# Optimization experiments

Measured on AMD Instinct MI355X. Metric: run time of the kernel, lower is better.

Reference implementation:

```python
import jax, jax.numpy as jnp
import numpy as np

B, T, I, H, L = 32, 512, 512, 512, 2


def gru_dir(x, w_ih, w_hh, b_ih, b_hh):
    """Single-direction GRU over x: [B, T, In] -> [B, T, H]. PyTorch gate order r,z,n."""
    Bb = x.shape[0]
    Hh = w_hh.shape[-1]
    # Fuse input-gate matmuls across all timesteps: [B, T, 3H]
    gx = jnp.einsum('bti,gi->btg', x, w_ih) + b_ih
    gx = jnp.moveaxis(gx, 1, 0)  # [T, B, 3H] for scan

    def step(h, gx_t):
        gh = h @ w_hh.T + b_hh  # [B, 3H]
        xr, xz, xn = jnp.split(gx_t, 3, axis=-1)
        hr, hz, hn = jnp.split(gh, 3, axis=-1)
        r = jax.nn.sigmoid(xr + hr)
        z = jax.nn.sigmoid(xz + hz)
        n = jnp.tanh(xn + r * hn)
        h_new = (1.0 - z) * n + z * h
        return h_new, h_new

    h0 = jnp.zeros((Bb, Hh), x.dtype)
    _, ys = jax.lax.scan(step, h0, gx)
    return jnp.moveaxis(ys, 0, 1)  # [B, T, H]


def bigru_layer(x, w_ih, w_hh, b_ih, b_hh):
    """w_ih: [2, 3H, In]; dir 0 = forward, dir 1 = backward (time-reversed)."""
    fwd = gru_dir(x, w_ih[0], w_hh[0], b_ih[0], b_hh[0])
    bwd = gru_dir(x[:, ::-1], w_ih[1], w_hh[1], b_ih[1], b_hh[1])[:, ::-1]
    return jnp.concatenate([fwd, bwd], axis=-1)  # [B, T, 2H]


def setup_inputs() -> dict:
    key = jax.random.key(0)
    ks = jax.random.split(key, 9)
    k = 1.0 / np.sqrt(H)  # PyTorch default uniform init bound
    u = lambda kk, shape: jax.random.uniform(kk, shape, jnp.float32, -k, k)
    x = jax.random.normal(ks[0], (B, T, I), jnp.float32)
    # Layer 0: input dim I; Layer 1: input dim 2H (bidirectional concat)
    return {
        'x': x,
        'w_ih_l0': u(ks[1], (2, 3 * H, I)),
        'w_hh_l0': u(ks[2], (2, 3 * H, H)),
        'b_ih_l0': u(ks[3], (2, 3 * H)),
        'b_hh_l0': u(ks[4], (2, 3 * H)),
        'w_ih_l1': u(ks[5], (2, 3 * H, 2 * H)),
        'w_hh_l1': u(ks[6], (2, 3 * H, H)),
        'b_ih_l1': u(ks[7], (2, 3 * H)),
        'b_hh_l1': u(ks[8], (2, 3 * H)),
    }


def reference(x, w_ih_l0, w_hh_l0, b_ih_l0, b_hh_l0,
              w_ih_l1, w_hh_l1, b_ih_l1, b_hh_l1):
    h1 = bigru_layer(x, w_ih_l0, w_hh_l0, b_ih_l0[:, None, :].squeeze(1), b_hh_l0)
    out = bigru_layer(h1, w_ih_l1, w_hh_l1, b_ih_l1, b_hh_l1)
    return out  # [B, T, 2H]
```

## Files before the change

kernel.cpp:

```cpp
#include <hip/hip_runtime.h>
#include <hip/hip_bf16.h>
#include <stdint.h>

#define TT 512
#define HD 512
#define BB 32
#define MM (BB*TT)
#define NG 3072
#define WGD 16
#define CPW 32

typedef short short8 __attribute__((ext_vector_type(8)));
typedef float f32x4 __attribute__((ext_vector_type(4)));
typedef float f32x2 __attribute__((ext_vector_type(2)));
typedef unsigned short u16;
typedef unsigned int u32;
typedef unsigned long long u64;

__device__ __forceinline__ u16 f2bf(float f) {
  __hip_bfloat16 h = __float2bfloat16(f);
  union { __hip_bfloat16 h; u16 u; } c; c.h = h; return c.u;
}
__device__ __forceinline__ float bf2f(u16 u) {
  union { u32 i; float f; } c; c.i = ((u32)u) << 16; return c.f;
}
__device__ __forceinline__ float sigmf(float x) {
  return 1.0f / (1.0f + __expf(-x));
}
__device__ __forceinline__ float tanhff(float x) {
  float a = __expf(2.0f * x);
  return 1.0f - 2.0f / (a + 1.0f);
}

__global__ __launch_bounds__(256) void cvt_bf16(const float* __restrict__ in,
                                                u16* __restrict__ out, int n8) {
  int i = blockIdx.x * 256 + threadIdx.x;
  if (i >= n8) return;
  const float4* p = (const float4*)in;
  float4 a = p[2*i], b = p[2*i+1];
  union { short8 v; u16 u[8]; } o;
  o.u[0]=f2bf(a.x); o.u[1]=f2bf(a.y); o.u[2]=f2bf(a.z); o.u[3]=f2bf(a.w);
  o.u[4]=f2bf(b.x); o.u[5]=f2bf(b.y); o.u[6]=f2bf(b.z); o.u[7]=f2bf(b.w);
  ((short8*)out)[i] = o.v;
}

__global__ __launch_bounds__(256) void gemm_gx(const u16* __restrict__ A,
                                               const u16* __restrict__ Bw,
                                               char* __restrict__ gxout,
                                               int K, int gxf32) {
  __shared__ __align__(16) u16 lA[128*32];
  __shared__ __align__(16) u16 lB[128*32];
  const int tid = threadIdx.x;
  const int lane = tid & 63;
  const int wid = tid >> 6;
  const int wr = wid >> 1, wc = wid & 1;
  const int bm = blockIdx.y * 128, bn = blockIdx.x * 128;
  const int col = lane & 15, kg = lane >> 4;

  f32x4 acc[4][4];
#pragma unroll
  for (int m = 0; m < 4; ++m)
#pragma unroll
    for (int n = 0; n < 4; ++n) acc[m][n] = (f32x4){0.f,0.f,0.f,0.f};

  const int nkt = K >> 5;
  for (int kt = 0; kt < nkt; ++kt) {
    short8 ra[2], rb[2];
    const int kb = kt * 32;
#pragma unroll
    for (int p = 0; p < 2; ++p) {
      int id = p*256 + tid;
      int row = id >> 2, c = id & 3;
      ra[p] = *(const short8*)(A  + (size_t)(bm+row)*K + kb + c*8);
      rb[p] = *(const short8*)(Bw + (size_t)(bn+row)*K + kb + c*8);
    }
    __syncthreads();
#pragma unroll
    for (int p = 0; p < 2; ++p) {
      int id = p*256 + tid;
      int row = id >> 2, c = id & 3;
      int off = row*64 + ((c ^ ((row>>1)&3))*16);
      *(short8*)((char*)lA + off) = ra[p];
      *(short8*)((char*)lB + off) = rb[p];
    }
    __syncthreads();
    short8 af[4], bf[4];
#pragma unroll
    for (int m = 0; m < 4; ++m) {
      int row = wr*64 + m*16 + col;
      af[m] = *(short8*)((char*)lA + row*64 + ((kg ^ ((row>>1)&3))*16));
    }
#pragma unroll
    for (int n = 0; n < 4; ++n) {
      int row = wc*64 + n*16 + col;
      bf[n] = *(short8*)((char*)lB + row*64 + ((kg ^ ((row>>1)&3))*16));
    }
#pragma unroll
    for (int m = 0; m < 4; ++m)
#pragma unroll
      for (int n = 0; n < 4; ++n)
        acc[m][n] = __builtin_amdgcn_mfma_f32_16x16x32_bf16(af[m], bf[n], acc[m][n], 0,0,0);
  }
#pragma unroll
  for (int m = 0; m < 4; ++m)
#pragma unroll
    for (int n = 0; n < 4; ++n)
#pragma unroll
      for (int r = 0; r < 4; ++r) {
        int rowg = bm + wr*64 + m*16 + kg*4 + r;
        int colg = bn + wc*64 + n*16 + col;
        float v = acc[m][n][r];
        if (gxf32) ((float*)gxout)[(size_t)rowg*NG + colg] = v;
        else       ((u16*)gxout)[(size_t)rowg*NG + colg] = f2bf(v);
      }
}

__global__ __launch_bounds__(512, 2) void bigru_rec(const char* __restrict__ gx,
                                                    const u16* __restrict__ whhb,
                                                    const float* __restrict__ b_ih,
                                                    const float* __restrict__ b_hh,
                                                    char* __restrict__ out,
                                                    u16* __restrict__ himg,
                                                    u32* __restrict__ flags,
                                                    int gxf32, int outf32) {
  const int wg = blockIdx.x;
  const int dir = wg >> 4;
  const int jb = wg & 15;
  const int tid = threadIdx.x;
  const int lane = tid & 63;
  const int wv = tid >> 6;
  const int col = lane & 15, kg = lane >> 4;

  __shared__ __align__(16) u16 hstage[32*512];
  __shared__ float gh[3][32][33];
  __shared__ __align__(16) char gxmem[2][12288];
  __shared__ float bihs[3][32], bhhs[3][32];
  __shared__ u32 lctr;

  short8 bfrag[16];
  if (wv < 6) {
    const int g = wv >> 1, ch = wv & 1;
    const u16* wrow = whhb + (size_t)(dir*1536 + g*512 + jb*CPW + ch*16 + col) * 512;
#pragma unroll
    for (int kc = 0; kc < 16; ++kc)
      bfrag[kc] = *(const short8*)(wrow + kc*32 + kg*8);
  }
  if (tid < 96) {
    int g = tid >> 5, j = tid & 31;
    bihs[g][j] = b_ih[dir*1536 + g*512 + jb*CPW + j];
    bhhs[g][j] = b_hh[dir*1536 + g*512 + jb*CPW + j];
  }
  if (tid == 0) lctr = 0;
  __syncthreads();

  const int gb = tid >> 4, gj0 = (tid & 15) * 2;
  float hp0 = 0.f, hp1 = 0.f;

  u32* dirflags = flags + (size_t)dir * WGD * 16;
  u32* myflag = dirflags + (size_t)jb * 16;

  for (int t = 0; t < TT; ++t) {
    const int tt = dir ? (TT - 1 - t) : t;
    const int par = t & 1;
    float* gxlF = (float*)gxmem[par];
    u16*   gxlB = (u16*)gxmem[par];

    if (gxf32) {
      const float* gxf = (const float*)gx;
      { int cid = tid; int b = cid/24, rem = cid%24, g = rem>>3, q = rem&7;
        float4 v = *(const float4*)(gxf + (size_t)(b*TT+tt)*NG + dir*1536 + g*512 + jb*CPW + q*4);
        *(float4*)&gxlF[g*1024 + b*32 + q*4] = v; }
      if (tid < 256) {
        int cid = 512 + tid; int b = cid/24, rem = cid%24, g = rem>>3, q = rem&7;
        float4 v = *(const float4*)(gxf + (size_t)(b*TT+tt)*NG + dir*1536 + g*512 + jb*CPW + q*4);
        *(float4*)&gxlF[g*1024 + b*32 + q*4] = v; }
    } else {
      if (tid < 384) {
        const u16* gxb = (const u16*)gx;
        int b = tid/12, rem = tid%12, g = rem>>2, q = rem&3;
        short8 v = *(const short8*)(gxb + (size_t)(b*TT+tt)*NG + dir*1536 + g*512 + jb*CPW + q*8);
        *(short8*)&gxlB[g*1024 + b*32 + q*8] = v;
      }
    }

    if (t > 0 && wv == 0) {
      const u32 need = (u32)t;
      const u32* fp = dirflags + (size_t)lane * 16;
      int iter = 0;
      while (iter++ < (1 << 24)) {
        u32 v = (lane < WGD)
              ? __hip_atomic_load(fp, __ATOMIC_RELAXED, __HIP_MEMORY_SCOPE_AGENT)
              : need;
        if (__all(v >= need)) break;
      }
    }
    __syncthreads();

    const u64* imgr = (const u64*)(himg + ((size_t)dir*2 + par) * 32 * 512);
#pragma unroll
    for (int p = 0; p < 8; ++p) {
      int id = p*512 + tid;
      int row = id >> 7, d2 = id & 127;
      u64 hv = __hip_atomic_load(imgr + row*128 + d2, __ATOMIC_RELAXED, __HIP_MEMORY_SCOPE_AGENT);
      int c = d2 >> 1;
      *(u64*)((char*)hstage + row*1024 + (((c ^ (row & 7)) << 4) | ((d2 & 1) << 3))) = hv;
    }
    __syncthreads();

    if (wv < 6) {
      const int g = wv >> 1, ch = wv & 1;
      f32x4 acc0 = (f32x4){0.f,0.f,0.f,0.f};
      f32x4 acc1 = (f32x4){0.f,0.f,0.f,0.f};
#pragma unroll
      for (int kc = 0; kc < 16; ++kc) {
        int c = kc*4 + kg;
        short8 a0 = *(short8*)((char*)hstage + col*1024      + ((c ^ (col & 7)) << 4));
        short8 a1 = *(short8*)((char*)hstage + (16+col)*1024 + ((c ^ (col & 7)) << 4));
        acc0 = __builtin_amdgcn_mfma_f32_16x16x32_bf16(a0, bfrag[kc], acc0, 0,0,0);
        acc1 = __builtin_amdgcn_mfma_f32_16x16x32_bf16(a1, bfrag[kc], acc1, 0,0,0);
      }
#pragma unroll
      for (int r = 0; r < 4; ++r) {
        gh[g][kg*4 + r][ch*16 + col]      = acc0[r];
        gh[g][16 + kg*4 + r][ch*16 + col] = acc1[r];
      }
    }
    __syncthreads();

    float hv0, hv1; u32 pv;
    {
      float xr0, xz0, xn0, xr1, xz1, xn1;
      if (gxf32) {
        xr0 = gxlF[gb*32+gj0];        xz0 = gxlF[1024+gb*32+gj0];   xn0 = gxlF[2048+gb*32+gj0];
        xr1 = gxlF[gb*32+gj0+1];      xz1 = gxlF[1024+gb*32+gj0+1]; xn1 = gxlF[2048+gb*32+gj0+1];
      } else {
        xr0 = bf2f(gxlB[gb*32+gj0]);   xz0 = bf2f(gxlB[1024+gb*32+gj0]);   xn0 = bf2f(gxlB[2048+gb*32+gj0]);
        xr1 = bf2f(gxlB[gb*32+gj0+1]); xz1 = bf2f(gxlB[1024+gb*32+gj0+1]); xn1 = bf2f(gxlB[2048+gb*32+gj0+1]);
      }
      float r0 = sigmf(xr0 + bihs[0][gj0]   + gh[0][gb][gj0]   + bhhs[0][gj0]);
      float z0 = sigmf(xz0 + bihs[1][gj0]   + gh[1][gb][gj0]   + bhhs[1][gj0]);
      float n0 = tanhff(xn0 + bihs[2][gj0]  + r0*(gh[2][gb][gj0] + bhhs[2][gj0]));
      hv0 = (1.f - z0)*n0 + z0*hp0;
      float r1 = sigmf(xr1 + bihs[0][gj0+1] + gh[0][gb][gj0+1] + bhhs[0][gj0+1]);
      float z1 = sigmf(xz1 + bihs[1][gj0+1] + gh[1][gb][gj0+1] + bhhs[1][gj0+1]);
      float n1 = tanhff(xn1 + bihs[2][gj0+1] + r1*(gh[2][gb][gj0+1] + bhhs[2][gj0+1]));
      hv1 = (1.f - z1)*n1 + z1*hp1;
      hp0 = hv0; hp1 = hv1;

      u32* img2 = (u32*)(himg + ((size_t)dir*2 + ((t + 1) & 1)) * 32 * 512);
      pv = (u32)f2bf(hv0) | ((u32)f2bf(hv1) << 16);
      __hip_atomic_store(img2 + gb*256 + jb*16 + (tid & 15), pv,
                         __ATOMIC_RELAXED, __HIP_MEMORY_SCOPE_AGENT);
    }

    asm volatile("s_waitcnt vmcnt(0)" ::: "memory");
    if (lane == 0) {
      u32 old = atomicAdd(&lctr, 1u);
      if (old == (u32)(t*8 + 7))
        __hip_atomic_store(myflag, (u32)(t + 1), __ATOMIC_RELAXED, __HIP_MEMORY_SCOPE_AGENT);
    }

    {
      size_t oi = (size_t)(gb*TT + tt)*1024 + dir*512 + jb*CPW + gj0;
      if (outf32) {
        f32x2 ov; ov.x = hv0; ov.y = hv1;
        __builtin_nontemporal_store(ov, (f32x2*)((float*)out + oi));
      } else {
        __builtin_nontemporal_store(pv, (u32*)((u16*)out + oi));
      }
    }
  }
}

extern "C" void kernel_launch(void* const* d_in, const int* in_sizes, int n_in,
                              void* d_out, int out_size, void* d_ws, size_t ws_size,
                              hipStream_t stream) {
  (void)in_sizes; (void)n_in; (void)out_size;
  const float* x    = (const float*)d_in[0];
  const float* wih0 = (const float*)d_in[1];
  const float* whh0 = (const float*)d_in[2];
  const float* bih0 = (const float*)d_in[3];
  const float* bhh0 = (const float*)d_in[4];
  const float* wih1 = (const float*)d_in[5];
  const float* whh1 = (const float*)d_in[6];
  const float* bih1 = (const float*)d_in[7];
  const float* bhh1 = (const float*)d_in[8];

  char* ws = (char*)d_ws;
  size_t off = 0;
  auto alloc = [&](size_t bytes) { size_t o = off; off += (bytes + 255) & ~(size_t)255; return o; };
  size_t off_xb   = alloc((size_t)MM * 512 * 2);
  size_t off_wih0 = alloc((size_t)3072 * 512 * 2);
  size_t off_wih1 = alloc((size_t)3072 * 1024 * 2);
  size_t off_whh0 = alloc((size_t)3072 * 512 * 2);
  size_t off_whh1 = alloc((size_t)3072 * 512 * 2);
  size_t off_h0   = alloc((size_t)MM * 1024 * 2);
  size_t off_sync = alloc(131072 + 4096);
  size_t off_gx   = off;
  int gxf32 = (ws_size >= off_gx + (size_t)MM * NG * 4) ? 1 : 0;

  u16* xb    = (u16*)(ws + off_xb);
  u16* wih0b = (u16*)(ws + off_wih0);
  u16* wih1b = (u16*)(ws + off_wih1);
  u16* whh0b = (u16*)(ws + off_whh0);
  u16* whh1b = (u16*)(ws + off_whh1);
  u16* h0b   = (u16*)(ws + off_h0);
  u16* himg  = (u16*)(ws + off_sync);
  u32* flags = (u32*)(ws + off_sync + 131072);
  char* gx   = ws + off_gx;

  cvt_bf16<<<4096, 256, 0, stream>>>(x,    xb,    MM*512/8);
  cvt_bf16<<<768,  256, 0, stream>>>(wih0, wih0b, 3072*512/8);
  cvt_bf16<<<1536, 256, 0, stream>>>(wih1, wih1b, 3072*1024/8);
  cvt_bf16<<<768,  256, 0, stream>>>(whh0, whh0b, 3072*512/8);
  cvt_bf16<<<768,  256, 0, stream>>>(whh1, whh1b, 3072*512/8);

  dim3 ggrid(NG/128, MM/128);

  gemm_gx<<<ggrid, 256, 0, stream>>>(xb, wih0b, gx, 512, gxf32);
  (void)hipMemsetAsync(ws + off_sync, 0, 131072 + 4096, stream);
  bigru_rec<<<32, 512, 0, stream>>>(gx, whh0b, bih0, bhh0, (char*)h0b, himg, flags, gxf32, 0);

  gemm_gx<<<ggrid, 256, 0, stream>>>(h0b, wih1b, gx, 1024, gxf32);
  (void)hipMemsetAsync(ws + off_sync, 0, 131072 + 4096, stream);
  bigru_rec<<<32, 512, 0, stream>>>(gx, whh1b, bih1, bhh1, (char*)d_out, himg, flags, gxf32, 1);
}
```

Before: 5.074 ms.

## Replace global flag barrier with per-producer waits and direct h-slice loads

Before, wave 0 spun until all 16 producer workgroups had posted their flags, then a block barrier ran, and only after that did every thread load the hidden-state image. Now each wave waits only on the flags of the two producer workgroups whose h columns it loads, and fetches those columns as soon as each flag is seen. One __syncthreads per step is removed. The gx prefetch is held in registers and written to LDS after the h loads, so global latency overlaps. The cost is that all eight waves now poll flags at once, which adds atomic traffic, and more registers are live.

New measurement: 4.662 ms. 1.09x faster.

```diff
diff --git a/kernel.cpp b/kernel.cpp
--- a/kernel.cpp
+++ b/kernel.cpp
@@ -159,51 +159,73 @@
   u32* dirflags = flags + (size_t)dir * WGD * 16;
   u32* myflag = dirflags + (size_t)jb * 16;
 
+  const int srow = lane >> 1, sg4 = (lane & 1) * 4;
+  const int p0 = wv, p1 = wv + 8;
+  const u32* fp0 = dirflags + (size_t)p0 * 16;
+  const u32* fp1 = dirflags + (size_t)p1 * 16;
+
   for (int t = 0; t < TT; ++t) {
     const int tt = dir ? (TT - 1 - t) : t;
     const int par = t & 1;
     float* gxlF = (float*)gxmem[par];
     u16*   gxlB = (u16*)gxmem[par];
 
+    float4 g0, g1; short8 gb16;
+    int c0_b=0,c0_g=0,c0_q=0, c1_b=0,c1_g=0,c1_q=0;
+    int b16_b=0,b16_g=0,b16_q=0;
     if (gxf32) {
       const float* gxf = (const float*)gx;
-      { int cid = tid; int b = cid/24, rem = cid%24, g = rem>>3, q = rem&7;
-        float4 v = *(const float4*)(gxf + (size_t)(b*TT+tt)*NG + dir*1536 + g*512 + jb*CPW + q*4);
-        *(float4*)&gxlF[g*1024 + b*32 + q*4] = v; }
+      { int cid = tid;      c0_b=cid/24; int r=cid%24; c0_g=r>>3; c0_q=r&7;
+        g0 = *(const float4*)(gxf + (size_t)(c0_b*TT+tt)*NG + dir*1536 + c0_g*512 + jb*CPW + c0_q*4); }
       if (tid < 256) {
-        int cid = 512 + tid; int b = cid/24, rem = cid%24, g = rem>>3, q = rem&7;
-        float4 v = *(const float4*)(gxf + (size_t)(b*TT+tt)*NG + dir*1536 + g*512 + jb*CPW + q*4);
-        *(float4*)&gxlF[g*1024 + b*32 + q*4] = v; }
+        int cid = 512+tid;  c1_b=cid/24; int r=cid%24; c1_g=r>>3; c1_q=r&7;
+        g1 = *(const float4*)(gxf + (size_t)(c1_b*TT+tt)*NG + dir*1536 + c1_g*512 + jb*CPW + c1_q*4); }
     } else {
       if (tid < 384) {
         const u16* gxb = (const u16*)gx;
-        int b = tid/12, rem = tid%12, g = rem>>2, q = rem&3;
-        short8 v = *(const short8*)(gxb + (size_t)(b*TT+tt)*NG + dir*1536 + g*512 + jb*CPW + q*8);
-        *(short8*)&gxlB[g*1024 + b*32 + q*8] = v;
-      }
-    }
-
-    if (t > 0 && wv == 0) {
+        b16_b = tid/12; int r = tid%12; b16_g = r>>2; b16_q = r&3;
+        gb16 = *(const short8*)(gxb + (size_t)(b16_b*TT+tt)*NG + dir*1536 + b16_g*512 + jb*CPW + b16_q*8);
+      }
+    }
+
+    const u64* imgr = (const u64*)(himg + ((size_t)dir*2 + par) * 32 * 512);
+    u64 v0[4], v1[4];
+    if (t > 0) {
       const u32 need = (u32)t;
-      const u32* fp = dirflags + (size_t)lane * 16;
-      int iter = 0;
-      while (iter++ < (1 << 24)) {
-        u32 v = (lane < WGD)
-              ? __hip_atomic_load(fp, __ATOMIC_RELAXED, __HIP_MEMORY_SCOPE_AGENT)
-              : need;
-        if (__all(v >= need)) break;
-      }
-    }
-    __syncthreads();
-
-    const u64* imgr = (const u64*)(himg + ((size_t)dir*2 + par) * 32 * 512);
-#pragma unroll
-    for (int p = 0; p < 8; ++p) {
-      int id = p*512 + tid;
-      int row = id >> 7, d2 = id & 127;
-      u64 hv = __hip_atomic_load(imgr + row*128 + d2, __ATOMIC_RELAXED, __HIP_MEMORY_SCOPE_AGENT);
-      int c = d2 >> 1;
-      *(u64*)((char*)hstage + row*1024 + (((c ^ (row & 7)) << 4) | ((d2 & 1) << 3))) = hv;
+      int it = 0;
+      while (__hip_atomic_load(fp0, __ATOMIC_RELAXED, __HIP_MEMORY_SCOPE_AGENT) < need && it++ < (1<<24)) {}
+    }
+    __builtin_amdgcn_sched_barrier(0);
+    asm volatile("" ::: "memory");
+#pragma unroll
+    for (int j = 0; j < 4; ++j)
+      v0[j] = __hip_atomic_load(imgr + srow*128 + p0*8 + sg4 + j, __ATOMIC_RELAXED, __HIP_MEMORY_SCOPE_AGENT);
+    if (t > 0) {
+      const u32 need = (u32)t;
+      int it = 0;
+      while (__hip_atomic_load(fp1, __ATOMIC_RELAXED, __HIP_MEMORY_SCOPE_AGENT) < need && it++ < (1<<24)) {}
+    }
+    __builtin_amdgcn_sched_barrier(0);
+    asm volatile("" ::: "memory");
+#pragma unroll
+    for (int j = 0; j < 4; ++j)
+      v1[j] = __hip_atomic_load(imgr + srow*128 + p1*8 + sg4 + j, __ATOMIC_RELAXED, __HIP_MEMORY_SCOPE_AGENT);
+
+#pragma unroll
+    for (int j = 0; j < 4; ++j) {
+      int d2 = p0*8 + sg4 + j; int c = d2 >> 1;
+      *(u64*)((char*)hstage + srow*1024 + (((c ^ (srow & 7)) << 4) | ((d2 & 1) << 3))) = v0[j];
+    }
+#pragma unroll
+    for (int j = 0; j < 4; ++j) {
+      int d2 = p1*8 + sg4 + j; int c = d2 >> 1;
+      *(u64*)((char*)hstage + srow*1024 + (((c ^ (srow & 7)) << 4) | ((d2 & 1) << 3))) = v1[j];
+    }
+    if (gxf32) {
+      *(float4*)&gxlF[c0_g*1024 + c0_b*32 + c0_q*4] = g0;
+      if (tid < 256) *(float4*)&gxlF[c1_g*1024 + c1_b*32 + c1_q*4] = g1;
+    } else {
+      if (tid < 384) *(short8*)&gxlB[b16_g*1024 + b16_b*32 + b16_q*8] = gb16;
     }
     __syncthreads();
 
```

## Load hidden-state MFMA fragments directly from global, drop LDS staging

Applied to the files above, without the earlier changes.

The recurrent kernel no longer stages the previous hidden state through a swizzled LDS buffer. Each MFMA wave now spins on the cross-workgroup flags itself and loads its A fragments straight from the global h image into registers. The gx prefetch buffer in LDS is also replaced by each thread loading its own six gate inputs into registers, and launch bounds move to one block per CU. This removes two __syncthreads and an LDS round trip from the per-step critical path, at the cost of redundant global loads across waves and higher register pressure.

Result: slower. 13.20 ms (+160.2%).

```diff
diff --git a/kernel.cpp b/kernel.cpp
--- a/kernel.cpp
+++ b/kernel.cpp
@@ -115,7 +115,7 @@
       }
 }
 
-__global__ __launch_bounds__(512, 2) void bigru_rec(const char* __restrict__ gx,
+__global__ __launch_bounds__(512, 1) void bigru_rec(const char* __restrict__ gx,
                                                     const u16* __restrict__ whhb,
                                                     const float* __restrict__ b_ih,
                                                     const float* __restrict__ b_hh,
@@ -131,9 +131,7 @@
   const int wv = tid >> 6;
   const int col = lane & 15, kg = lane >> 4;
 
-  __shared__ __align__(16) u16 hstage[32*512];
   __shared__ float gh[3][32][33];
-  __shared__ __align__(16) char gxmem[2][12288];
   __shared__ float bihs[3][32], bhhs[3][32];
   __shared__ u32 lctr;
 
@@ -162,62 +160,56 @@
   for (int t = 0; t < TT; ++t) {
     const int tt = dir ? (TT - 1 - t) : t;
     const int par = t & 1;
-    float* gxlF = (float*)gxmem[par];
-    u16*   gxlB = (u16*)gxmem[par];
-
+
+    f32x2 xrF, xzF, xnF; u32 xrB=0, xzB=0, xnB=0;
     if (gxf32) {
-      const float* gxf = (const float*)gx;
-      { int cid = tid; int b = cid/24, rem = cid%24, g = rem>>3, q = rem&7;
-        float4 v = *(const float4*)(gxf + (size_t)(b*TT+tt)*NG + dir*1536 + g*512 + jb*CPW + q*4);
-        *(float4*)&gxlF[g*1024 + b*32 + q*4] = v; }
-      if (tid < 256) {
-        int cid = 512 + tid; int b = cid/24, rem = cid%24, g = rem>>3, q = rem&7;
-        float4 v = *(const float4*)(gxf + (size_t)(b*TT+tt)*NG + dir*1536 + g*512 + jb*CPW + q*4);
-        *(float4*)&gxlF[g*1024 + b*32 + q*4] = v; }
+      const float* gp = (const float*)gx + (size_t)(gb*TT+tt)*NG + dir*1536 + jb*CPW + gj0;
+      xrF = *(const f32x2*)(gp);
+      xzF = *(const f32x2*)(gp + 512);
+      xnF = *(const f32x2*)(gp + 1024);
     } else {
-      if (tid < 384) {
-        const u16* gxb = (const u16*)gx;
-        int b = tid/12, rem = tid%12, g = rem>>2, q = rem&3;
-        short8 v = *(const short8*)(gxb + (size_t)(b*TT+tt)*NG + dir*1536 + g*512 + jb*CPW + q*8);
-        *(short8*)&gxlB[g*1024 + b*32 + q*8] = v;
-      }
-    }
-
-    if (t > 0 && wv == 0) {
-      const u32 need = (u32)t;
-      const u32* fp = dirflags + (size_t)lane * 16;
-      int iter = 0;
-      while (iter++ < (1 << 24)) {
-        u32 v = (lane < WGD)
-              ? __hip_atomic_load(fp, __ATOMIC_RELAXED, __HIP_MEMORY_SCOPE_AGENT)
-              : need;
-        if (__all(v >= need)) break;
-      }
-    }
-    __syncthreads();
-
-    const u64* imgr = (const u64*)(himg + ((size_t)dir*2 + par) * 32 * 512);
-#pragma unroll
-    for (int p = 0; p < 8; ++p) {
-      int id = p*512 + tid;
-      int row = id >> 7, d2 = id & 127;
-      u64 hv = __hip_atomic_load(imgr + row*128 + d2, __ATOMIC_RELAXED, __HIP_MEMORY_SCOPE_AGENT);
-      int c = d2 >> 1;
-      *(u64*)((char*)hstage + row*1024 + (((c ^ (row & 7)) << 4) | ((d2 & 1) << 3))) = hv;
-    }
-    __syncthreads();
+      const u16* gp = (const u16*)gx + (size_t)(gb*TT+tt)*NG + dir*1536 + jb*CPW + gj0;
+      xrB = *(const u32*)(gp);
+      xzB = *(const u32*)(gp + 512);
+      xnB = *(const u32*)(gp + 1024);
+    }
 
     if (wv < 6) {
+      if (t > 0) {
+        const u32 need = (u32)t;
+        const u32* fp = dirflags + (size_t)lane * 16;
+        int it = 0;
+        while (it++ < (1 << 24)) {
+          u32 v = (lane < WGD)
+                ? __hip_atomic_load(fp, __ATOMIC_RELAXED, __HIP_MEMORY_SCOPE_AGENT)
+                : (u32)t;
+          if (__all(v >= need)) break;
+        }
+      }
+      __builtin_amdgcn_sched_barrier(0);
+      asm volatile("" ::: "memory");
+
+      const u64* imgq = (const u64*)(himg + ((size_t)dir*2 + par) * 32 * 512);
+      u64 fa[16][2][2];
+#pragma unroll
+      for (int kc = 0; kc < 16; ++kc)
+#pragma unroll
+        for (int m = 0; m < 2; ++m)
+#pragma unroll
+          for (int h = 0; h < 2; ++h)
+            fa[kc][m][h] = __hip_atomic_load(imgq + (m*16 + col)*128 + kc*8 + kg*2 + h,
+                                             __ATOMIC_RELAXED, __HIP_MEMORY_SCOPE_AGENT);
+
       const int g = wv >> 1, ch = wv & 1;
       f32x4 acc0 = (f32x4){0.f,0.f,0.f,0.f};
       f32x4 acc1 = (f32x4){0.f,0.f,0.f,0.f};
 #pragma unroll
       for (int kc = 0; kc < 16; ++kc) {
-        int c = kc*4 + kg;
-        short8 a0 = *(short8*)((char*)hstage + col*1024      + ((c ^ (col & 7)) << 4));
-        short8 a1 = *(short8*)((char*)hstage + (16+col)*1024 + ((c ^ (col & 7)) << 4));
-        acc0 = __builtin_amdgcn_mfma_f32_16x16x32_bf16(a0, bfrag[kc], acc0, 0,0,0);
-        acc1 = __builtin_amdgcn_mfma_f32_16x16x32_bf16(a1, bfrag[kc], acc1, 0,0,0);
+        union { u64 q[2]; short8 s; } a0, a1;
+        a0.q[0] = fa[kc][0][0]; a0.q[1] = fa[kc][0][1];
+        a1.q[0] = fa[kc][1][0]; a1.q[1] = fa[kc][1][1];
+        acc0 = __builtin_amdgcn_mfma_f32_16x16x32_bf16(a0.s, bfrag[kc], acc0, 0,0,0);
+        acc1 = __builtin_amdgcn_mfma_f32_16x16x32_bf16(a1.s, bfrag[kc], acc1, 0,0,0);
       }
 #pragma unroll
       for (int r = 0; r < 4; ++r) {
@@ -231,11 +223,11 @@
     {
       float xr0, xz0, xn0, xr1, xz1, xn1;
       if (gxf32) {
-        xr0 = gxlF[gb*32+gj0];        xz0 = gxlF[1024+gb*32+gj0];   xn0 = gxlF[2048+gb*32+gj0];
-        xr1 = gxlF[gb*32+gj0+1];      xz1 = gxlF[1024+gb*32+gj0+1]; xn1 = gxlF[2048+gb*32+gj0+1];
+        xr0 = xrF.x; xz0 = xzF.x; xn0 = xnF.x;
+        xr1 = xrF.y; xz1 = xzF.y; xn1 = xnF.y;
       } else {
-        xr0 = bf2f(gxlB[gb*32+gj0]);   xz0 = bf2f(gxlB[1024+gb*32+gj0]);   xn0 = bf2f(gxlB[2048+gb*32+gj0]);
-        xr1 = bf2f(gxlB[gb*32+gj0+1]); xz1 = bf2f(gxlB[1024+gb*32+gj0+1]); xn1 = bf2f(gxlB[2048+gb*32+gj0+1]);
+        xr0 = bf2f((u16)(xrB & 0xffff)); xz0 = bf2f((u16)(xzB & 0xffff)); xn0 = bf2f((u16)(xnB & 0xffff));
+        xr1 = bf2f((u16)(xrB >> 16));    xz1 = bf2f((u16)(xzB >> 16));    xn1 = bf2f((u16)(xnB >> 16));
       }
       float r0 = sigmf(xr0 + bihs[0][gj0]   + gh[0][gb][gj0]   + bhhs[0][gj0]);
       float z0 = sigmf(xz0 + bihs[1][gj0]   + gh[1][gb][gj0]   + bhhs[1][gj0]);
```
